# Kernel tuning notes

Hardware: AMD Instinct MI355X
Metric: run time of the kernel (lower is better)

The kernel has to match this reference:

```python
import jax, jax.numpy as jnp
import numpy as np

DIM = 2048
K = 4

def setup_inputs() -> dict:
    key = jax.random.key(0)
    k1, k2, k3 = jax.random.split(key, 3)
    x = jax.random.normal(k1, (4, 4096, DIM), dtype=jnp.float32)
    # torch Conv1d(dim, dim, K, groups=dim): weight [D,1,K] -> store as [D,K]; bias [D]
    bound = 1.0 / np.sqrt(K)  # fan_in = (in_channels/groups)*K = K
    w = jax.random.uniform(k2, (DIM, K), dtype=jnp.float32, minval=-bound, maxval=bound)
    b = jax.random.uniform(k3, (DIM,), dtype=jnp.float32, minval=-bound, maxval=bound)
    return {"x": x, "w": w, "b": b}

def reference(x, w, b):
    # Causal depthwise conv1d on [B,S,D]: out[t,d] = b[d] + sum_k w[d,k]*x[t+k-(K-1),d]
    B, S, D = x.shape
    xp = jnp.pad(x, ((0, 0), (K - 1, 0), (0, 0)))  # left-pad time axis
    y = b  # broadcasts over [B,S,D]
    for k in range(K):  # small fixed kernel loop (K=4)
        y = y + xp[:, k:k + S, :] * w[:, k]
    return y
```

## Files before the change

kernel.cpp:

```cpp
#include <hip/hip_runtime.h>

#define DIM    2048
#define SEQ    4096
#define BATCH  4
#define KW     4
#define TCHUNK 16

typedef float fvec4 __attribute__((ext_vector_type(4)));

__global__ __launch_bounds__(256) void ShortConv1D_78855599554935_kernel(
    const float* __restrict__ x, const float* __restrict__ w,
    const float* __restrict__ bias, float* __restrict__ out)
{
    constexpr int D4 = DIM / 4;
    constexpr int NT = SEQ / TCHUNK;

    int idx  = blockIdx.x * blockDim.x + threadIdx.x;
    int d4   = idx & (D4 - 1);
    int rest = idx >> 9;
    int tc   = rest & (NT - 1);
    int bb   = rest >> 8;

    const fvec4* __restrict__ x4 = (const fvec4*)x;
    const fvec4* __restrict__ w4 = (const fvec4*)w;
    const fvec4* __restrict__ b4 = (const fvec4*)bias;
    fvec4* __restrict__ o4 = (fvec4*)out;

    long base = ((long)bb * SEQ + (long)tc * TCHUNK) * D4 + d4;

    fvec4 xv[TCHUNK + 3];
    if (tc > 0) {
        xv[0] = x4[base - 3 * D4];
        xv[1] = x4[base - 2 * D4];
        xv[2] = x4[base - 1 * D4];
    } else {
        xv[0] = (fvec4)(0.f);
        xv[1] = (fvec4)(0.f);
        xv[2] = (fvec4)(0.f);
    }
#pragma unroll
    for (int t = 0; t < TCHUNK; ++t) {
        xv[3 + t] = x4[base + t * D4];
    }

    fvec4 w0 = w4[d4 * 4 + 0];
    fvec4 w1 = w4[d4 * 4 + 1];
    fvec4 w2 = w4[d4 * 4 + 2];
    fvec4 w3 = w4[d4 * 4 + 3];
    fvec4 bv = b4[d4];

#pragma unroll
    for (int t = 0; t < TCHUNK; ++t) {
        fvec4 a  = xv[t];
        fvec4 bq = xv[t + 1];
        fvec4 c  = xv[t + 2];
        fvec4 dd = xv[t + 3];
        fvec4 r;
        r.x = bv.x + w0.x * a.x + w0.y * bq.x + w0.z * c.x + w0.w * dd.x;
        r.y = bv.y + w1.x * a.y + w1.y * bq.y + w1.z * c.y + w1.w * dd.y;
        r.z = bv.z + w2.x * a.z + w2.y * bq.z + w2.z * c.z + w2.w * dd.z;
        r.w = bv.w + w3.x * a.w + w3.y * bq.w + w3.z * c.w + w3.w * dd.w;
        o4[base + t * D4] = r;
    }
}

extern "C" void kernel_launch(void* const* d_in, const int* in_sizes, int n_in,
                              void* d_out, int out_size, void* d_ws, size_t ws_size,
                              hipStream_t stream) {
    const float* x = (const float*)d_in[0];
    const float* w = (const float*)d_in[1];
    const float* b = (const float*)d_in[2];
    float* out = (float*)d_out;

    constexpr int D4 = DIM / 4;
    constexpr int NT = SEQ / TCHUNK;
    int total_threads = BATCH * NT * D4;
    int block = 256;
    int grid = total_threads / block;

    ShortConv1D_78855599554935_kernel<<<grid, block, 0, stream>>>(x, w, b, out);
}
```

Measured before the change: 238.5 us.

## Process longer time segments per thread with double-buffered register chunks

Each thread now covers a 64-step time segment instead of 16 steps. It loads 8-row chunks into two alternating register buffers so the next chunk's loads are issued while the current chunk is computed and stored. The three-row halo is carried in registers between chunks, which cuts redundant halo reads and the per-thread setup of weights and bias. The trade-off is four times fewer threads in the grid, so less parallelism is available to hide memory latency.

```diff
diff --git a/kernel.cpp b/kernel.cpp
--- a/kernel.cpp
+++ b/kernel.cpp
@@ -4,44 +4,32 @@
 #define SEQ    4096
 #define BATCH  4
 #define KW     4
-#define TCHUNK 16
+#define TCHUNK 8
+#define SEGLEN 64
 
 typedef float fvec4 __attribute__((ext_vector_type(4)));
 
-__global__ __launch_bounds__(256) void ShortConv1D_78855599554935_kernel(
+constexpr int D4      = DIM / 4;
+constexpr int NSEG    = SEQ / SEGLEN;
+constexpr int NTHREAD = BATCH * NSEG * D4;
+constexpr int BLOCKSZ = 256;
+constexpr int NBLOCK  = NTHREAD / BLOCKSZ;
+constexpr int ITERS   = SEGLEN / TCHUNK;
+
+__global__ __launch_bounds__(BLOCKSZ) void ShortConv1D_78855599554935_kernel(
     const float* __restrict__ x, const float* __restrict__ w,
     const float* __restrict__ bias, float* __restrict__ out)
 {
-    constexpr int D4 = DIM / 4;
-    constexpr int NT = SEQ / TCHUNK;
-
-    int idx  = blockIdx.x * blockDim.x + threadIdx.x;
-    int d4   = idx & (D4 - 1);
-    int rest = idx >> 9;
-    int tc   = rest & (NT - 1);
-    int bb   = rest >> 8;
+    int idx = blockIdx.x * BLOCKSZ + threadIdx.x;
+    int d4  = idx & (D4 - 1);
+    int r   = idx >> 9;
+    int seg = r & (NSEG - 1);
+    int bb  = r >> 6;
 
     const fvec4* __restrict__ x4 = (const fvec4*)x;
     const fvec4* __restrict__ w4 = (const fvec4*)w;
     const fvec4* __restrict__ b4 = (const fvec4*)bias;
     fvec4* __restrict__ o4 = (fvec4*)out;
-
-    long base = ((long)bb * SEQ + (long)tc * TCHUNK) * D4 + d4;
-
-    fvec4 xv[TCHUNK + 3];
-    if (tc > 0) {
-        xv[0] = x4[base - 3 * D4];
-        xv[1] = x4[base - 2 * D4];
-        xv[2] = x4[base - 1 * D4];
-    } else {
-        xv[0] = (fvec4)(0.f);
-        xv[1] = (fvec4)(0.f);
-        xv[2] = (fvec4)(0.f);
-    }
-#pragma unroll
-    for (int t = 0; t < TCHUNK; ++t) {
-        xv[3 + t] = x4[base + t * D4];
-    }
 
     fvec4 w0 = w4[d4 * 4 + 0];
     fvec4 w1 = w4[d4 * 4 + 1];
@@ -49,19 +37,58 @@
     fvec4 w3 = w4[d4 * 4 + 3];
     fvec4 bv = b4[d4];
 
+    long tseg = (long)seg * SEGLEN;
+    long base = ((long)bb * SEQ + tseg) * D4 + d4;
+
+    fvec4 h0, h1, h2;
+    if (seg > 0) {
+        h0 = x4[base - 3 * D4];
+        h1 = x4[base - 2 * D4];
+        h2 = x4[base - 1 * D4];
+    } else {
+        h0 = (fvec4)(0.f);
+        h1 = (fvec4)(0.f);
+        h2 = (fvec4)(0.f);
+    }
+
+    fvec4 bufA[TCHUNK], bufB[TCHUNK];
+
+#define LOADCH(buf, t4)                                                       \
+    do {                                                                      \
+        _Pragma("unroll")                                                     \
+        for (int j = 0; j < TCHUNK; ++j) (buf)[j] = x4[(t4) + j * D4];        \
+    } while (0)
+
+#define COMPST(buf, t4)                                                       \
+    do {                                                                      \
+        fvec4 v0 = h0, v1 = h1, v2 = h2;                                      \
+        _Pragma("unroll")                                                     \
+        for (int j = 0; j < TCHUNK; ++j) {                                    \
+            fvec4 dd = (buf)[j];                                              \
+            fvec4 rr;                                                         \
+            rr.x = bv.x + w0.x * v0.x + w0.y * v1.x + w0.z * v2.x + w0.w * dd.x; \
+            rr.y = bv.y + w1.x * v0.y + w1.y * v1.y + w1.z * v2.y + w1.w * dd.y; \
+            rr.z = bv.z + w2.x * v0.z + w2.y * v1.z + w2.z * v2.z + w2.w * dd.z; \
+            rr.w = bv.w + w3.x * v0.w + w3.y * v1.w + w3.z * v2.w + w3.w * dd.w; \
+            o4[(t4) + j * D4] = rr;                                           \
+            v0 = v1; v1 = v2; v2 = dd;                                        \
+        }                                                                     \
+        h0 = v0; h1 = v1; h2 = v2;                                            \
+    } while (0)
+
+    LOADCH(bufA, base);
 #pragma unroll
-    for (int t = 0; t < TCHUNK; ++t) {
-        fvec4 a  = xv[t];
-        fvec4 bq = xv[t + 1];
-        fvec4 c  = xv[t + 2];
-        fvec4 dd = xv[t + 3];
-        fvec4 r;
-        r.x = bv.x + w0.x * a.x + w0.y * bq.x + w0.z * c.x + w0.w * dd.x;
-        r.y = bv.y + w1.x * a.y + w1.y * bq.y + w1.z * c.y + w1.w * dd.y;
-        r.z = bv.z + w2.x * a.z + w2.y * bq.z + w2.z * c.z + w2.w * dd.z;
-        r.w = bv.w + w3.x * a.w + w3.y * bq.w + w3.z * c.w + w3.w * dd.w;
-        o4[base + t * D4] = r;
+    for (int it = 0; it < ITERS; it += 2) {
+        long tA = base + (long)it * TCHUNK * D4;
+        long tB = tA + TCHUNK * D4;
+        if (it + 1 < ITERS) LOADCH(bufB, tB);
+        COMPST(bufA, tA);
+        if (it + 2 < ITERS) LOADCH(bufA, tB + TCHUNK * D4);
+        if (it + 1 < ITERS) COMPST(bufB, tB);
     }
+
+#undef LOADCH
+#undef COMPST
 }
 
 extern "C" void kernel_launch(void* const* d_in, const int* in_sizes, int n_in,
@@ -72,11 +99,5 @@
     const float* b = (const float*)d_in[2];
     float* out = (float*)d_out;
 
-    constexpr int D4 = DIM / 4;
-    constexpr int NT = SEQ / TCHUNK;
-    int total_threads = BATCH * NT * D4;
-    int block = 256;
-    int grid = total_threads / block;
-
-    ShortConv1D_78855599554935_kernel<<<grid, block, 0, stream>>>(x, w, b, out);
+    ShortConv1D_78855599554935_kernel<<<NBLOCK, BLOCKSZ, 0, stream>>>(x, w, b, out);
 }
```

New measurement: 239.6 us. No clear change (+0.5%).

## Replace per-thread time chunks with grid-stride loop reloading halo rows

Applied to the files above, without the earlier changes.

Each thread previously computed a 16-step time chunk held in registers. Now a fixed grid of 1024 blocks loops over rows with a stride, and for every output row it loads the current row plus three previous rows directly from global memory. This aims to reduce register pressure and the launch size, and to improve latency hiding through the loop. In exchange, global load requests grow roughly fourfold, relying on cache hits for the reused neighbouring rows.

```diff
diff --git a/kernel.cpp b/kernel.cpp
--- a/kernel.cpp
+++ b/kernel.cpp
@@ -4,44 +4,29 @@
 #define SEQ    4096
 #define BATCH  4
 #define KW     4
-#define TCHUNK 16
 
 typedef float fvec4 __attribute__((ext_vector_type(4)));
 
-__global__ __launch_bounds__(256) void ShortConv1D_78855599554935_kernel(
+constexpr int  D4      = DIM / 4;
+constexpr long TOTAL4  = (long)BATCH * SEQ * D4;
+constexpr int  BLOCKSZ = 256;
+constexpr int  NBLOCK  = 1024;
+constexpr int  NTHREAD = NBLOCK * BLOCKSZ;
+constexpr int  ITERS   = (int)(TOTAL4 / NTHREAD);
+
+__global__ __launch_bounds__(BLOCKSZ) void ShortConv1D_78855599554935_kernel(
     const float* __restrict__ x, const float* __restrict__ w,
     const float* __restrict__ bias, float* __restrict__ out)
 {
-    constexpr int D4 = DIM / 4;
-    constexpr int NT = SEQ / TCHUNK;
-
-    int idx  = blockIdx.x * blockDim.x + threadIdx.x;
-    int d4   = idx & (D4 - 1);
-    int rest = idx >> 9;
-    int tc   = rest & (NT - 1);
-    int bb   = rest >> 8;
+    int tid = blockIdx.x * BLOCKSZ + threadIdx.x;
+    int d4  = tid & (D4 - 1);
+    int row0 = tid >> 9;
+    constexpr int ROWSTEP = NTHREAD >> 9;
 
     const fvec4* __restrict__ x4 = (const fvec4*)x;
     const fvec4* __restrict__ w4 = (const fvec4*)w;
     const fvec4* __restrict__ b4 = (const fvec4*)bias;
     fvec4* __restrict__ o4 = (fvec4*)out;
-
-    long base = ((long)bb * SEQ + (long)tc * TCHUNK) * D4 + d4;
-
-    fvec4 xv[TCHUNK + 3];
-    if (tc > 0) {
-        xv[0] = x4[base - 3 * D4];
-        xv[1] = x4[base - 2 * D4];
-        xv[2] = x4[base - 1 * D4];
-    } else {
-        xv[0] = (fvec4)(0.f);
-        xv[1] = (fvec4)(0.f);
-        xv[2] = (fvec4)(0.f);
-    }
-#pragma unroll
-    for (int t = 0; t < TCHUNK; ++t) {
-        xv[3 + t] = x4[base + t * D4];
-    }
 
     fvec4 w0 = w4[d4 * 4 + 0];
     fvec4 w1 = w4[d4 * 4 + 1];
@@ -49,18 +34,30 @@
     fvec4 w3 = w4[d4 * 4 + 3];
     fvec4 bv = b4[d4];
 
-#pragma unroll
-    for (int t = 0; t < TCHUNK; ++t) {
-        fvec4 a  = xv[t];
-        fvec4 bq = xv[t + 1];
-        fvec4 c  = xv[t + 2];
-        fvec4 dd = xv[t + 3];
+#pragma unroll 2
+    for (int it = 0; it < ITERS; ++it) {
+        int  row = row0 + it * ROWSTEP;
+        int  t   = row & (SEQ - 1);
+        long g   = ((long)row << 9) | d4;
+
+        fvec4 dd = x4[g];
+        fvec4 a, bq, c;
+        if (t >= 3) {
+            c  = x4[g - 1 * D4];
+            bq = x4[g - 2 * D4];
+            a  = x4[g - 3 * D4];
+        } else {
+            c  = (t >= 1) ? x4[g - 1 * D4] : (fvec4)(0.f);
+            bq = (t >= 2) ? x4[g - 2 * D4] : (fvec4)(0.f);
+            a  = (fvec4)(0.f);
+        }
+
         fvec4 r;
         r.x = bv.x + w0.x * a.x + w0.y * bq.x + w0.z * c.x + w0.w * dd.x;
         r.y = bv.y + w1.x * a.y + w1.y * bq.y + w1.z * c.y + w1.w * dd.y;
         r.z = bv.z + w2.x * a.z + w2.y * bq.z + w2.z * c.z + w2.w * dd.z;
         r.w = bv.w + w3.x * a.w + w3.y * bq.w + w3.z * c.w + w3.w * dd.w;
-        o4[base + t * D4] = r;
+        o4[g] = r;
     }
 }
 
@@ -72,11 +69,5 @@
     const float* b = (const float*)d_in[2];
     float* out = (float*)d_out;
 
-    constexpr int D4 = DIM / 4;
-    constexpr int NT = SEQ / TCHUNK;
-    int total_threads = BATCH * NT * D4;
-    int block = 256;
-    int grid = total_threads / block;
-
-    ShortConv1D_78855599554935_kernel<<<grid, block, 0, stream>>>(x, w, b, out);
+    ShortConv1D_78855599554935_kernel<<<NBLOCK, BLOCKSZ, 0, stream>>>(x, w, b, out);
 }
```

Result: slower. 255.7 us (+7.2%).
